# Performance work log

Hardware: AMD Instinct MI355X
Metric: run time of the kernel (lower is better)

## Reference

```python
import jax, jax.numpy as jnp
import numpy as np

B, H, W, C = 4, 64, 64, 256
CD = C // 8

def setup_inputs() -> dict:
    key = jax.random.key(0)
    ks = jax.random.split(key, 4)
    x = jax.random.normal(ks[0], (B, H, W, C), dtype=jnp.float32)
    Wf = jax.random.normal(ks[1], (C, CD), dtype=jnp.float32) * (1.0 / np.sqrt(C))
    Wg = jax.random.normal(ks[2], (C, CD), dtype=jnp.float32) * (1.0 / np.sqrt(C))
    Wh = jax.random.normal(ks[3], (C, C), dtype=jnp.float32) * (1.0 / np.sqrt(C))
    bf = jnp.zeros((CD,), dtype=jnp.float32)
    bg = jnp.zeros((CD,), dtype=jnp.float32)
    bh = jnp.zeros((C,), dtype=jnp.float32)
    return {"x": x, "Wf": Wf, "bf": bf, "Wg": Wg, "bg": bg, "Wh": Wh, "bh": bh}

def reference(x, Wf, bf, Wg, bg, Wh, bh):
    b, h, w, c = x.shape
    n = h * w
    xf = x.reshape(b, n, c)                       # [B,N,C]
    f = xf @ Wf + bf                              # [B,N,C/8] (1x1 conv == per-token linear)
    g = xf @ Wg + bg                              # [B,N,C/8]
    hh = xf @ Wh + bh                             # [B,N,C]
    s = jnp.einsum('bnd,bmd->bnm', g, f)          # g @ f^T, unscaled
    attn = jax.nn.softmax(s, axis=-1)             # [B,N,N]
    o = jnp.einsum('bnm,bmc->bnc', attn, hh)      # [B,N,C]
    return x + o.reshape(b, h, w, c)
```

## Files before the change

kernel.cpp:

```cpp
#include <hip/hip_runtime.h>
#include <hip/hip_bf16.h>
#include <stdint.h>

#define NN 4096
#define CC 256
#define DD 32
#define CHW 17408
#define NCT 9

typedef short    bf16x8 __attribute__((ext_vector_type(8)));
typedef _Float16 f16x8  __attribute__((ext_vector_type(8)));
typedef float    f32x4  __attribute__((ext_vector_type(4)));

__device__ __forceinline__ unsigned short bf16_rne(float x) {
    union { float f; unsigned int u; } v; v.f = x;
    unsigned int u = v.u;
    return (unsigned short)((u + 0x7FFFu + ((u >> 16) & 1u)) >> 16);
}
__device__ __forceinline__ float bf16f(unsigned short h) {
    union { float f; unsigned int u; } v; v.u = ((unsigned int)h) << 16; return v.f;
}
__device__ __forceinline__ unsigned short f16_bits(float x) {
    union { _Float16 h; unsigned short u; } v; v.h = (_Float16)x;
    return v.u;
}
__device__ __forceinline__ unsigned int cvt_pk_bf16(float lo, float hi) {
    unsigned int r;
    asm("v_cvt_pk_bf16_f32 %0, %1, %2" : "=v"(r) : "v"(lo), "v"(hi));
    return r;
}
__device__ __forceinline__ void load_lds16(const unsigned short* g, unsigned short* l) {
    __builtin_amdgcn_global_load_lds(
        (const __attribute__((address_space(1))) unsigned int*)g,
        (__attribute__((address_space(3))) unsigned int*)l, 16, 0, 0);
}

__global__ __launch_bounds__(256) void prep_kernel(
    const float* __restrict__ Wf, const float* __restrict__ Wg,
    const float* __restrict__ Wh, unsigned short* __restrict__ Wst)
{
    int id  = blockIdx.x * 256 + threadIdx.x;
    int ks  = id / 12288;
    int rem = id - ks * 12288;
    int row = rem >> 5;
    int k   = ks * 32 + (rem & 31);
    unsigned short outv;
    if (row < 256) {
        outv = bf16_rne(Wh[(size_t)k * CC + row]);
    } else if (row < 320) {
        int d = row - 256;
        float v = (d < 32) ? Wf[(size_t)k * DD + d] : Wg[(size_t)k * DD + (d - 32)];
        outv = bf16_rne(v);
    } else {
        int d = row - 320;
        float v = (d < 32) ? Wf[(size_t)k * DD + d] : Wg[(size_t)k * DD + (d - 32)];
        unsigned short h = bf16_rne(v);
        outv = bf16_rne(v - bf16f(h));
    }
    Wst[id] = outv;
}

__global__ __launch_bounds__(256, 2) void proj_kernel(
    const float* __restrict__ x,
    const float* __restrict__ bfv, const float* __restrict__ bgv,
    const float* __restrict__ bhv,
    const unsigned short* __restrict__ Wst,
    unsigned short* __restrict__ f16b, unsigned short* __restrict__ g16b,
    unsigned short* __restrict__ hhT)
{
    const int tid  = threadIdx.x;
    const int lane = tid & 63;
    const int wv   = tid >> 6;
    const int col  = lane & 15;
    const int quad = lane >> 4;
    const int tok0 = blockIdx.x * 32;
    const int b    = tok0 >> 12;

    __shared__ __align__(16) unsigned short xh[32 * 272];
    __shared__ __align__(16) unsigned short xl[32 * 272];
    __shared__ __align__(16) unsigned short WT[1920 * 8];

    #pragma unroll
    for (int it = 0; it < 8; ++it) {
        int idx = it * 1024 + tid * 4;
        float4 v = *(const float4*)(x + (size_t)tok0 * CC + idx);
        int tok = idx >> 8, k = idx & 255;
        unsigned short h0 = bf16_rne(v.x), h1 = bf16_rne(v.y),
                       h2 = bf16_rne(v.z), h3 = bf16_rne(v.w);
        uint2 wh_, wl_;
        wh_.x = (unsigned int)h0 | ((unsigned int)h1 << 16);
        wh_.y = (unsigned int)h2 | ((unsigned int)h3 << 16);
        wl_.x = (unsigned int)bf16_rne(v.x - bf16f(h0)) |
                ((unsigned int)bf16_rne(v.y - bf16f(h1)) << 16);
        wl_.y = (unsigned int)bf16_rne(v.z - bf16f(h2)) |
                ((unsigned int)bf16_rne(v.w - bf16f(h3)) << 16);
        *(uint2*)&xh[tok * 272 + k] = wh_;
        *(uint2*)&xl[tok * 272 + k] = wl_;
    }

    f32x4 acc[5][2];
    #pragma unroll
    for (int t = 0; t < 5; ++t) {
        int tl = wv * 5 + t;
        float bias;
        if (tl < 16) bias = bhv[tl * 16 + col];
        else { int fd = (tl - 16) * 16 + col;
               bias = (fd < 32) ? bfv[fd] : bgv[fd - 32]; }
        acc[t][0] = (f32x4){bias, bias, bias, bias};
        acc[t][1] = (f32x4){bias, bias, bias, bias};
    }

    for (int ks = 0; ks < 8; ++ks) {
        for (int t = 0; t < 8; ++t) {
            int i = wv + t * 4;
            if (i >= 30) break;
            int l = i * 64 + lane;
            int row = l / 5, g = l - row * 5;
            const unsigned short* gp = (g < 4)
                ? (Wst + (size_t)ks * 12288 + row * 32 + g * 8)
                : (Wst + (size_t)ks * 12288);
            load_lds16(gp, &WT[i * 512]);
        }
        __syncthreads();

        bf16x8 ah[2], al[2];
        #pragma unroll
        for (int mt = 0; mt < 2; ++mt) {
            ah[mt] = *(const bf16x8*)&xh[(mt * 16 + col) * 272 + ks * 32 + quad * 8];
            al[mt] = *(const bf16x8*)&xl[(mt * 16 + col) * 272 + ks * 32 + quad * 8];
        }

        #pragma unroll
        for (int t = 0; t < 5; ++t) {
            int tl = wv * 5 + t;
            int wrow = (tl < 16) ? (tl * 16 + col) : (256 + (tl - 16) * 16 + col);
            bf16x8 bh = *(const bf16x8*)&WT[wrow * 40 + quad * 8];
            #pragma unroll
            for (int mt = 0; mt < 2; ++mt) {
                acc[t][mt] = __builtin_amdgcn_mfma_f32_16x16x32_bf16(ah[mt], bh, acc[t][mt], 0, 0, 0);
                acc[t][mt] = __builtin_amdgcn_mfma_f32_16x16x32_bf16(al[mt], bh, acc[t][mt], 0, 0, 0);
            }
            if (tl >= 16) {
                bf16x8 bl = *(const bf16x8*)&WT[(wrow + 64) * 40 + quad * 8];
                #pragma unroll
                for (int mt = 0; mt < 2; ++mt)
                    acc[t][mt] = __builtin_amdgcn_mfma_f32_16x16x32_bf16(ah[mt], bl, acc[t][mt], 0, 0, 0);
            }
        }
        __syncthreads();
    }

    const int ks_h = (tok0 & 63) >> 5;
    const int kc   = (tok0 & 4095) >> 6;
    const size_t tbase = ((size_t)(b * 64 + kc)) * CHW;
    #pragma unroll
    for (int t = 0; t < 5; ++t) {
        int tl = wv * 5 + t;
        if (tl < 16) {
            #pragma unroll
            for (int mt = 0; mt < 2; ++mt) {
                int qk = mt * 2 + (quad >> 1);
                int jb = (quad & 1) * 4;
                uint2 w;
                w.x = (unsigned int)bf16_rne(acc[t][mt][0]) | ((unsigned int)bf16_rne(acc[t][mt][1]) << 16);
                w.y = (unsigned int)bf16_rne(acc[t][mt][2]) | ((unsigned int)bf16_rne(acc[t][mt][3]) << 16);
                *(uint2*)&hhT[tbase + (size_t)(((ks_h * 17 + tl) * 64) + qk * 16 + col) * 8 + jb] = w;
            }
        } else {
            int fd = (tl - 16) * 16 + col;
            unsigned short* dst = (fd < 32) ? f16b : g16b;
            int d = fd & 31;
            #pragma unroll
            for (int mt = 0; mt < 2; ++mt)
                #pragma unroll
                for (int r = 0; r < 4; ++r) {
                    int tok = tok0 + mt * 16 + quad * 4 + r;
                    dst[(size_t)tok * DD + d] = f16_bits(acc[t][mt][r]);
                }
        }
    }
    #pragma unroll
    for (int it = 0; it < 2; ++it) {
        int e = tid + it * 256;
        int j = e & 7, ck = (e >> 3) & 15, qk = e >> 7;
        hhT[tbase + (size_t)(((ks_h * 17 + 16) * 64) + qk * 16 + ck) * 8 + j] =
            (ck == 0) ? (unsigned short)0x3F80 : (unsigned short)0;
    }
}

__global__ __launch_bounds__(256, 4) void attn_kernel(
    const unsigned short* __restrict__ g16b,
    const unsigned short* __restrict__ f16b,
    const unsigned short* __restrict__ hhT,
    unsigned short* __restrict__ Ob0,
    unsigned short* __restrict__ Ob1,
    unsigned short* __restrict__ Ob2,
    unsigned short* __restrict__ Ob3,
    float* __restrict__ lbuf)
{
    const int tid  = threadIdx.x;
    const int lane = tid & 63;
    const int wv   = tid >> 6;
    const int col  = lane & 15;
    const int quad = lane >> 4;
    const int bid  = blockIdx.x;
    const int csp  = bid & 1;
    const int sp   = (bid >> 1) & 3;
    const int b    = (bid >> 3) & 3;
    const int qblk = bid >> 5;
    const int q0   = qblk * 128 + wv * 32;
    const int kcb  = sp * 16;

    __shared__ __align__(16) unsigned short hbuf[2][NCT * 512];

    const unsigned short* fb16 = f16b + (size_t)b * NN * DD;
    const unsigned short* hb   = hhT + (size_t)b * 64 * CHW;

    f16x8 a_g[2];
    #pragma unroll
    for (int a = 0; a < 2; ++a)
        a_g[a] = *(const f16x8*)(g16b + ((size_t)(b * NN + q0 + a * 16 + col)) * DD + quad * 8);

    const int kpermu = (col >> 2) * 8 + (col & 3);

    const f32x4 m40 = {-40.f, -40.f, -40.f, -40.f};
    f32x4 acc[2][NCT];
    #pragma unroll
    for (int a = 0; a < 2; ++a)
        #pragma unroll
        for (int i = 0; i < NCT; ++i) acc[a][i] = (f32x4){0.f, 0.f, 0.f, 0.f};

    {
        const unsigned short* tile = hb + (size_t)kcb * CHW;
        #pragma unroll
        for (int t = 0; t < 3; ++t) {
            int s = wv + t * 4;
            if (s >= NCT) break;
            int ct = (s < 8) ? (csp * 8 + s) : 16;
            load_lds16(tile + (size_t)ct * 512 + lane * 8, &hbuf[0][s * 512]);
        }
    }
    __syncthreads();

    for (int hs = 0; hs < 32; ++hs) {
        const int nb = hs & 1;

        if (hs + 1 < 32) {
            const int kc = kcb + ((hs + 1) >> 1);
            const int ks = (hs + 1) & 1;
            const unsigned short* tile = hb + (size_t)kc * CHW + (size_t)(ks * 17) * 512;
            #pragma unroll
            for (int t = 0; t < 3; ++t) {
                int s = wv + t * 4;
                if (s >= NCT) break;
                int ct = (s < 8) ? (csp * 8 + s) : 16;
                load_lds16(tile + (size_t)ct * 512 + lane * 8, &hbuf[nb ^ 1][s * 512]);
            }
        }

        const int kk0 = kcb * 64 + hs * 32;

        f32x4 s_t[2][2];
        #pragma unroll
        for (int ktl = 0; ktl < 2; ++ktl) {
            f16x8 af_ = *(const f16x8*)(fb16 +
                (size_t)(kk0 + kpermu + ktl * 4) * DD + quad * 8);
            #pragma unroll
            for (int a = 0; a < 2; ++a)
                s_t[ktl][a] = __builtin_amdgcn_mfma_f32_16x16x32_f16(af_, a_g[a], m40, 0, 0, 0);
        }

        bf16x8 a_p[2];
        #pragma unroll
        for (int a = 0; a < 2; ++a) {
            union { unsigned int u[4]; bf16x8 v; } cv;
            #pragma unroll
            for (int ktl = 0; ktl < 2; ++ktl) {
                float e0 = __expf(s_t[ktl][a][0]);
                float e1 = __expf(s_t[ktl][a][1]);
                float e2 = __expf(s_t[ktl][a][2]);
                float e3 = __expf(s_t[ktl][a][3]);
                cv.u[ktl * 2 + 0] = cvt_pk_bf16(e0, e1);
                cv.u[ktl * 2 + 1] = cvt_pk_bf16(e2, e3);
            }
            a_p[a] = cv.v;
        }

        __builtin_amdgcn_sched_barrier(0);
        if (wv == 0) asm volatile("s_waitcnt vmcnt(3)" ::: "memory");
        else         asm volatile("s_waitcnt vmcnt(2)" ::: "memory");
        __builtin_amdgcn_s_barrier();
        __builtin_amdgcn_sched_barrier(0);

        __builtin_amdgcn_s_setprio(1);
        #pragma unroll
        for (int s = 0; s < NCT; ++s) {
            bf16x8 bh = *(const bf16x8*)&hbuf[nb][(s * 64 + lane) * 8];
            acc[0][s] = __builtin_amdgcn_mfma_f32_16x16x32_bf16(a_p[0], bh, acc[0][s], 0, 0, 0);
            acc[1][s] = __builtin_amdgcn_mfma_f32_16x16x32_bf16(a_p[1], bh, acc[1][s], 0, 0, 0);
        }
        __builtin_amdgcn_s_setprio(0);

        __builtin_amdgcn_sched_barrier(0);
        __builtin_amdgcn_s_barrier();
        __builtin_amdgcn_sched_barrier(0);
    }

    unsigned short* Obufs[4] = {Ob0, Ob1, Ob2, Ob3};
    unsigned short* Op = Obufs[sp];
    #pragma unroll
    for (int a = 0; a < 2; ++a) {
        const size_t obase = (size_t)(b * NN + q0 + a * 16) * CC;
        #pragma unroll
        for (int s = 0; s < 8; ++s) {
            const int ch = (csp * 8 + s) * 16 + col;
            #pragma unroll
            for (int r = 0; r < 4; ++r)
                Op[obase + (size_t)(quad * 4 + r) * CC + ch] = bf16_rne(acc[a][s][r]);
        }
        if (csp == 0 && col == 0) {
            #pragma unroll
            for (int r = 0; r < 4; ++r)
                lbuf[sp * (4 * NN) + b * NN + q0 + a * 16 + quad * 4 + r] = acc[a][8][r];
        }
    }
}

__global__ __launch_bounds__(256) void reduce_kernel(
    const float* __restrict__ x,
    const unsigned short* __restrict__ Ob0, const unsigned short* __restrict__ Ob1,
    const unsigned short* __restrict__ Ob2, const unsigned short* __restrict__ Ob3,
    const float* __restrict__ lbuf, float* __restrict__ out)
{
    int id = blockIdx.x * 256 + threadIdx.x;
    int q  = id >> 5;
    int c8 = (id & 31) * 8;
    size_t base = (size_t)q * CC + c8;
    float inv = 1.0f / (lbuf[q] + lbuf[4 * NN + q] + lbuf[8 * NN + q] + lbuf[12 * NN + q]);
    uint4 u0 = *(const uint4*)(Ob0 + base);
    uint4 u1 = *(const uint4*)(Ob1 + base);
    uint4 u2 = *(const uint4*)(Ob2 + base);
    uint4 u3 = *(const uint4*)(Ob3 + base);
    float4 xa = *(const float4*)(x + base);
    float4 xb = *(const float4*)(x + base + 4);
    float s[8];
    #pragma unroll
    for (int i = 0; i < 4; ++i) {
        unsigned int w0 = ((const unsigned int*)&u0)[i];
        unsigned int w1 = ((const unsigned int*)&u1)[i];
        unsigned int w2 = ((const unsigned int*)&u2)[i];
        unsigned int w3 = ((const unsigned int*)&u3)[i];
        s[2 * i]     = bf16f((unsigned short)w0) + bf16f((unsigned short)w1)
                     + bf16f((unsigned short)w2) + bf16f((unsigned short)w3);
        s[2 * i + 1] = bf16f((unsigned short)(w0 >> 16)) + bf16f((unsigned short)(w1 >> 16))
                     + bf16f((unsigned short)(w2 >> 16)) + bf16f((unsigned short)(w3 >> 16));
    }
    float4 ra, rb;
    ra.x = xa.x + s[0] * inv;
    ra.y = xa.y + s[1] * inv;
    ra.z = xa.z + s[2] * inv;
    ra.w = xa.w + s[3] * inv;
    rb.x = xb.x + s[4] * inv;
    rb.y = xb.y + s[5] * inv;
    rb.z = xb.z + s[6] * inv;
    rb.w = xb.w + s[7] * inv;
    *(float4*)(out + base) = ra;
    *(float4*)(out + base + 4) = rb;
}

extern "C" void kernel_launch(void* const* d_in, const int* in_sizes, int n_in,
                              void* d_out, int out_size, void* d_ws, size_t ws_size,
                              hipStream_t stream) {
    const float* x  = (const float*)d_in[0];
    const float* Wf = (const float*)d_in[1];
    const float* bf = (const float*)d_in[2];
    const float* Wg = (const float*)d_in[3];
    const float* bg = (const float*)d_in[4];
    const float* Wh = (const float*)d_in[5];
    const float* bh = (const float*)d_in[6];
    float* out = (float*)d_out;

    unsigned char* ws = (unsigned char*)d_ws;
    unsigned short* Wst  = (unsigned short*)(ws);
    unsigned short* f16b = (unsigned short*)(ws + 0x040000);
    unsigned short* g16b = (unsigned short*)(ws + 0x140000);
    unsigned short* hhT  = (unsigned short*)(ws + 0x240000);
    unsigned short* Ob0  = (unsigned short*)(ws + 0xAC0000);
    unsigned short* Ob1  = (unsigned short*)(ws + 0x12C0000);
    unsigned short* Ob2  = (unsigned short*)(ws + 0x1AC0000);
    unsigned short* Ob3  = (unsigned short*)(ws + 0x22C0000);
    float*          lbuf = (float*)(ws + 0x2AC0000);

    prep_kernel<<<384, 256, 0, stream>>>(Wf, Wg, Wh, Wst);
    proj_kernel<<<512, 256, 0, stream>>>(x, bf, bg, bh, Wst, f16b, g16b, hhT);
    attn_kernel<<<1024, 256, 0, stream>>>(g16b, f16b, hhT, Ob0, Ob1, Ob2, Ob3, lbuf);
    reduce_kernel<<<2048, 256, 0, stream>>>(x, Ob0, Ob1, Ob2, Ob3, lbuf, out);
}
```

Before: 148.1 us.

## Compute all output channels per block to stop recomputing attention scores

The attention kernel drops the split of output channels across two blocks. Each block now accumulates all 256 channels plus the row-sum column, so the QK scores and exponentials are computed once instead of twice, and the grid is halved. LDS staging grows to a full 64-key chunk per stage (two halves of 17 tiles), with one barrier per chunk instead of per half. Each wave now holds twice as many accumulators, so register pressure rises (launch bounds relaxed to 2) and occupancy drops, which may hurt latency hiding.

Result: faster. 142.4 us, median of 2 (-3.9%).

```diff
diff --git a/kernel.cpp b/kernel.cpp
--- a/kernel.cpp
+++ b/kernel.cpp
@@ -6,7 +6,6 @@
 #define CC 256
 #define DD 32
 #define CHW 17408
-#define NCT 9
 
 typedef short    bf16x8 __attribute__((ext_vector_type(8)));
 typedef _Float16 f16x8  __attribute__((ext_vector_type(8)));
@@ -188,7 +187,7 @@
     }
 }
 
-__global__ __launch_bounds__(256, 4) void attn_kernel(
+__global__ __launch_bounds__(256, 2) void attn_kernel(
     const unsigned short* __restrict__ g16b,
     const unsigned short* __restrict__ f16b,
     const unsigned short* __restrict__ hhT,
@@ -204,14 +203,13 @@
     const int col  = lane & 15;
     const int quad = lane >> 4;
     const int bid  = blockIdx.x;
-    const int csp  = bid & 1;
-    const int sp   = (bid >> 1) & 3;
-    const int b    = (bid >> 3) & 3;
-    const int qblk = bid >> 5;
+    const int sp   = bid & 3;
+    const int b    = (bid >> 2) & 3;
+    const int qblk = bid >> 4;
     const int q0   = qblk * 128 + wv * 32;
     const int kcb  = sp * 16;
 
-    __shared__ __align__(16) unsigned short hbuf[2][NCT * 512];
+    __shared__ __align__(16) unsigned short hbuf[2][34 * 512];
 
     const unsigned short* fb16 = f16b + (size_t)b * NN * DD;
     const unsigned short* hb   = hhT + (size_t)b * 64 * CHW;
@@ -224,86 +222,75 @@
     const int kpermu = (col >> 2) * 8 + (col & 3);
 
     const f32x4 m40 = {-40.f, -40.f, -40.f, -40.f};
-    f32x4 acc[2][NCT];
+    f32x4 acc[2][17];
     #pragma unroll
     for (int a = 0; a < 2; ++a)
         #pragma unroll
-        for (int i = 0; i < NCT; ++i) acc[a][i] = (f32x4){0.f, 0.f, 0.f, 0.f};
+        for (int i = 0; i < 17; ++i) acc[a][i] = (f32x4){0.f, 0.f, 0.f, 0.f};
 
     {
         const unsigned short* tile = hb + (size_t)kcb * CHW;
-        #pragma unroll
-        for (int t = 0; t < 3; ++t) {
-            int s = wv + t * 4;
-            if (s >= NCT) break;
-            int ct = (s < 8) ? (csp * 8 + s) : 16;
-            load_lds16(tile + (size_t)ct * 512 + lane * 8, &hbuf[0][s * 512]);
+        for (int t = 0; t < 9; ++t) {
+            int i = wv + t * 4;
+            if (i >= 34) break;
+            load_lds16(tile + (size_t)(i * 64 + lane) * 8, &hbuf[0][i * 512]);
         }
     }
     __syncthreads();
 
-    for (int hs = 0; hs < 32; ++hs) {
-        const int nb = hs & 1;
-
-        if (hs + 1 < 32) {
-            const int kc = kcb + ((hs + 1) >> 1);
-            const int ks = (hs + 1) & 1;
-            const unsigned short* tile = hb + (size_t)kc * CHW + (size_t)(ks * 17) * 512;
-            #pragma unroll
-            for (int t = 0; t < 3; ++t) {
-                int s = wv + t * 4;
-                if (s >= NCT) break;
-                int ct = (s < 8) ? (csp * 8 + s) : 16;
-                load_lds16(tile + (size_t)ct * 512 + lane * 8, &hbuf[nb ^ 1][s * 512]);
-            }
-        }
-
-        const int kk0 = kcb * 64 + hs * 32;
-
-        f32x4 s_t[2][2];
-        #pragma unroll
-        for (int ktl = 0; ktl < 2; ++ktl) {
-            f16x8 af_ = *(const f16x8*)(fb16 +
-                (size_t)(kk0 + kpermu + ktl * 4) * DD + quad * 8);
-            #pragma unroll
-            for (int a = 0; a < 2; ++a)
-                s_t[ktl][a] = __builtin_amdgcn_mfma_f32_16x16x32_f16(af_, a_g[a], m40, 0, 0, 0);
-        }
-
-        bf16x8 a_p[2];
-        #pragma unroll
-        for (int a = 0; a < 2; ++a) {
-            union { unsigned int u[4]; bf16x8 v; } cv;
+    for (int kc = 0; kc < 16; ++kc) {
+        const int nb = kc & 1;
+
+        if (kc + 1 < 16) {
+            const unsigned short* tile = hb + (size_t)(kcb + kc + 1) * CHW;
+            for (int t = 0; t < 9; ++t) {
+                int i = wv + t * 4;
+                if (i >= 34) break;
+                load_lds16(tile + (size_t)(i * 64 + lane) * 8, &hbuf[nb ^ 1][i * 512]);
+            }
+        }
+
+        #pragma unroll
+        for (int half = 0; half < 2; ++half) {
+            const int kk0 = (kcb + kc) * 64 + half * 32;
+
+            f32x4 s_t[2][2];
             #pragma unroll
             for (int ktl = 0; ktl < 2; ++ktl) {
-                float e0 = __expf(s_t[ktl][a][0]);
-                float e1 = __expf(s_t[ktl][a][1]);
-                float e2 = __expf(s_t[ktl][a][2]);
-                float e3 = __expf(s_t[ktl][a][3]);
-                cv.u[ktl * 2 + 0] = cvt_pk_bf16(e0, e1);
-                cv.u[ktl * 2 + 1] = cvt_pk_bf16(e2, e3);
-            }
-            a_p[a] = cv.v;
-        }
-
-        __builtin_amdgcn_sched_barrier(0);
-        if (wv == 0) asm volatile("s_waitcnt vmcnt(3)" ::: "memory");
-        else         asm volatile("s_waitcnt vmcnt(2)" ::: "memory");
-        __builtin_amdgcn_s_barrier();
-        __builtin_amdgcn_sched_barrier(0);
-
-        __builtin_amdgcn_s_setprio(1);
-        #pragma unroll
-        for (int s = 0; s < NCT; ++s) {
-            bf16x8 bh = *(const bf16x8*)&hbuf[nb][(s * 64 + lane) * 8];
-            acc[0][s] = __builtin_amdgcn_mfma_f32_16x16x32_bf16(a_p[0], bh, acc[0][s], 0, 0, 0);
-            acc[1][s] = __builtin_amdgcn_mfma_f32_16x16x32_bf16(a_p[1], bh, acc[1][s], 0, 0, 0);
-        }
-        __builtin_amdgcn_s_setprio(0);
-
-        __builtin_amdgcn_sched_barrier(0);
-        __builtin_amdgcn_s_barrier();
-        __builtin_amdgcn_sched_barrier(0);
+                f16x8 af_ = *(const f16x8*)(fb16 +
+                    (size_t)(kk0 + kpermu + ktl * 4) * DD + quad * 8);
+                #pragma unroll
+                for (int a = 0; a < 2; ++a)
+                    s_t[ktl][a] = __builtin_amdgcn_mfma_f32_16x16x32_f16(af_, a_g[a], m40, 0, 0, 0);
+            }
+
+            bf16x8 a_p[2];
+            #pragma unroll
+            for (int a = 0; a < 2; ++a) {
+                union { unsigned int u[4]; bf16x8 v; } cv;
+                #pragma unroll
+                for (int ktl = 0; ktl < 2; ++ktl) {
+                    float e0 = __expf(s_t[ktl][a][0]);
+                    float e1 = __expf(s_t[ktl][a][1]);
+                    float e2 = __expf(s_t[ktl][a][2]);
+                    float e3 = __expf(s_t[ktl][a][3]);
+                    cv.u[ktl * 2 + 0] = cvt_pk_bf16(e0, e1);
+                    cv.u[ktl * 2 + 1] = cvt_pk_bf16(e2, e3);
+                }
+                a_p[a] = cv.v;
+            }
+
+            __builtin_amdgcn_s_setprio(1);
+            #pragma unroll
+            for (int s = 0; s < 17; ++s) {
+                bf16x8 bh = *(const bf16x8*)&hbuf[nb][((half * 17 + s) * 64 + lane) * 8];
+                acc[0][s] = __builtin_amdgcn_mfma_f32_16x16x32_bf16(a_p[0], bh, acc[0][s], 0, 0, 0);
+                acc[1][s] = __builtin_amdgcn_mfma_f32_16x16x32_bf16(a_p[1], bh, acc[1][s], 0, 0, 0);
+            }
+            __builtin_amdgcn_s_setprio(0);
+        }
+
+        __syncthreads();
     }
 
     unsigned short* Obufs[4] = {Ob0, Ob1, Ob2, Ob3};
@@ -312,16 +299,16 @@
     for (int a = 0; a < 2; ++a) {
         const size_t obase = (size_t)(b * NN + q0 + a * 16) * CC;
         #pragma unroll
-        for (int s = 0; s < 8; ++s) {
-            const int ch = (csp * 8 + s) * 16 + col;
+        for (int s = 0; s < 16; ++s) {
+            const int ch = s * 16 + col;
             #pragma unroll
             for (int r = 0; r < 4; ++r)
                 Op[obase + (size_t)(quad * 4 + r) * CC + ch] = bf16_rne(acc[a][s][r]);
         }
-        if (csp == 0 && col == 0) {
+        if (col == 0) {
             #pragma unroll
             for (int r = 0; r < 4; ++r)
-                lbuf[sp * (4 * NN) + b * NN + q0 + a * 16 + quad * 4 + r] = acc[a][8][r];
+                lbuf[sp * (4 * NN) + b * NN + q0 + a * 16 + quad * 4 + r] = acc[a][16][r];
         }
     }
 }
@@ -393,6 +380,6 @@
 
     prep_kernel<<<384, 256, 0, stream>>>(Wf, Wg, Wh, Wst);
     proj_kernel<<<512, 256, 0, stream>>>(x, bf, bg, bh, Wst, f16b, g16b, hhT);
-    attn_kernel<<<1024, 256, 0, stream>>>(g16b, f16b, hhT, Ob0, Ob1, Ob2, Ob3, lbuf);
+    attn_kernel<<<512, 256, 0, stream>>>(g16b, f16b, hhT, Ob0, Ob1, Ob2, Ob3, lbuf);
     reduce_kernel<<<2048, 256, 0, stream>>>(x, Ob0, Ob1, Ob2, Ob3, lbuf, out);
 }
```
